# Performance work log

Hardware: AMD Instinct MI355X
Metric: run time of the kernel (lower is better)

## Reference

```python
import jax, jax.numpy as jnp
import numpy as np

B, D, C = 16384, 1024, 2048


def setup_inputs() -> dict:
    key = jax.random.key(0)
    k1, k2 = jax.random.split(key)
    x = jax.random.normal(k1, (B, D), dtype=jnp.float32)
    # xavier_uniform for centers of shape (C, D): bound = sqrt(6/(C+D))
    bound = float(np.sqrt(6.0 / (C + D)))
    centers = jax.random.uniform(k2, (C, D), dtype=jnp.float32, minval=-bound, maxval=bound)
    gamma = jnp.ones((1,), dtype=jnp.float32)
    return {"x": x, "centers": centers, "gamma": gamma}


def _rbf(x, centers, gamma):
    # then Euclidean norm (sqrt) and exp(-gamma * dist) as in the torch module.
    x2 = jnp.sum(x * x, axis=-1, keepdims=True)            # (B, 1)
    c2 = jnp.sum(centers * centers, axis=-1)               # (C,)
    sq = x2 - 2.0 * jnp.einsum('bd,cd->bc', x, centers) + c2[None, :]
    dist = jnp.sqrt(jnp.maximum(sq, 0.0))                  # (B, C)
    return jnp.exp(-gamma[0] * dist)


def reference(x, centers, gamma):
    return _rbf(x, centers, gamma)
```

## Files before the change

### kernel.cpp

```cpp
#include <hip/hip_runtime.h>
#include <stdint.h>


typedef __attribute__((ext_vector_type(4))) int i32x4;

#define BM 128
#define BN 128
#define BK 64

__global__ __launch_bounds__(256) void prep_i8(
    const float* __restrict__ in, unsigned char* __restrict__ qb,
    float2* __restrict__ info, int K) {
  int row = blockIdx.x;
  int tid = threadIdx.x;
  float4 v = ((const float4*)(in + (size_t)row * K))[tid];
  float ss = v.x * v.x + v.y * v.y + v.z * v.z + v.w * v.w;
  float am = fmaxf(fmaxf(fabsf(v.x), fabsf(v.y)), fmaxf(fabsf(v.z), fabsf(v.w)));
  for (int off = 32; off > 0; off >>= 1) {
    ss += __shfl_down(ss, off, 64);
    am = fmaxf(am, __shfl_down(am, off, 64));
  }
  __shared__ float pss[4], pam[4], sbc;
  int lane = tid & 63, w = tid >> 6;
  if (lane == 0) { pss[w] = ss; pam[w] = am; }
  __syncthreads();
  if (tid == 0) {
    float tss = pss[0] + pss[1] + pss[2] + pss[3];
    float tam = fmaxf(fmaxf(pam[0], pam[1]), fmaxf(pam[2], pam[3]));
    float s = tam > 0.f ? 127.f / tam : 0.f;
    info[row] = make_float2(tss, tam * (1.f / 127.f));
    sbc = s;
  }
  __syncthreads();
  float s = sbc;
  int qx = __float2int_rn(v.x * s), qy = __float2int_rn(v.y * s);
  int qz = __float2int_rn(v.z * s), qw = __float2int_rn(v.w * s);
  unsigned u = (unsigned)(qx & 255) | ((unsigned)(qy & 255) << 8) |
               ((unsigned)(qz & 255) << 16) | ((unsigned)(qw & 255) << 24);
  ((unsigned*)qb)[(size_t)row * (K >> 2) + tid] = u;
}

#define GLDS(gptr, lptr)                                                      \
  __builtin_amdgcn_global_load_lds(                                           \
      (const __attribute__((address_space(1))) unsigned int*)(gptr),          \
      (__attribute__((address_space(3))) unsigned int*)(lptr), 16, 0, 0)

#define DSR(dst, addr, imm)                                                   \
  asm volatile("ds_read_b128 %0, %1 offset:%c2"                              \
               : "=v"(dst) : "v"(addr), "i"(imm))

#define BARRIER __builtin_amdgcn_s_barrier()
#define LGKM0                                                                 \
  do {                                                                        \
    asm volatile("s_waitcnt lgkmcnt(0)" ::: "memory");                        \
    __builtin_amdgcn_sched_barrier(0);                                        \
  } while (0)
#define VMW(n) asm volatile("s_waitcnt vmcnt(" #n ")" ::: "memory")

#define MFMAI8(a, b, c) __builtin_amdgcn_mfma_i32_16x16x64_i8((a), (b), (c), 0, 0, 0)

__global__ __launch_bounds__(256) void rbf_gemm_i8(
    const unsigned char* __restrict__ A, const unsigned char* __restrict__ Bm,
    const float2* __restrict__ xinfo, const float2* __restrict__ cinfo,
    const float* __restrict__ gamma, float* __restrict__ out,
    int M, int N, int K) {
  __shared__ __align__(16) unsigned char lds[2 * 16384];

  int nbn = N / BN;
  int nwg = (M / BM) * nbn;
  int bid = blockIdx.x;
  int wg = bid;
  if ((nwg & 7) == 0) {
    int cpx = nwg >> 3;
    wg = (bid & 7) * cpx + (bid >> 3);
  }
  int bm = wg / nbn, bn = wg % nbn;

  int tid = threadIdx.x;
  int lane = tid & 63, wv = tid >> 6;
  int wm = wv >> 1;
  int wn = wv & 1;
  int l15 = lane & 15, l4 = lane >> 4;

  const size_t Kz = (size_t)K;

  int pr = tid >> 2;
  int lr = pr ^ ((pr >> 2) & 1);
  int ls = (tid & 3) ^ (lr & 3);
  const unsigned char* AgT = A + (size_t)bm * BM * Kz + (size_t)lr * Kz + ls * 16;
  const unsigned char* BgT = Bm + (size_t)bn * BN * Kz + (size_t)lr * Kz + ls * 16;
  size_t rstep = (size_t)64 * Kz;

#define STG4(TAU, BUFS)                                                       \
  do {                                                                        \
    GLDS(AgT + (size_t)(TAU) * 64, (BUFS) + tid * 16);                        \
    GLDS(AgT + rstep + (size_t)(TAU) * 64, (BUFS) + 4096 + tid * 16);         \
    GLDS(BgT + (size_t)(TAU) * 64, (BUFS) + 8192 + tid * 16);                 \
    GLDS(BgT + rstep + (size_t)(TAU) * 64, (BUFS) + 12288 + tid * 16);        \
  } while (0)

  int sl15 = l15 ^ ((l15 >> 2) & 1);
  int fsl = l4 ^ (l15 & 3);
  unsigned ldsBase =
      (unsigned)(size_t)(const __attribute__((address_space(3))) void*)&lds[0];
  unsigned aBase = ldsBase + (unsigned)(wm * 4096 + sl15 * 64 + fsl * 16);
  unsigned bBase = ldsBase + (unsigned)(8192 + wn * 4096 + sl15 * 64 + fsl * 16);

  i32x4 acc[4][4];
#pragma unroll
  for (int m = 0; m < 4; ++m)
#pragma unroll
    for (int n = 0; n < 4; ++n) acc[m][n] = (i32x4){0, 0, 0, 0};

  int nt = K / BK;

  STG4(0, lds);
  VMW(0);
  BARRIER;

  for (int t = 0; t < nt; ++t) {
    unsigned bufOff = (unsigned)(t & 1) * 16384u;
    unsigned char* bufS = lds + ((t + 1) & 1) * 16384;

    unsigned aAd = aBase + bufOff;
    unsigned bAd = bBase + bufOff;

    i32x4 a0, a1, a2, a3, b0, b1, b2, b3;
    DSR(a0, aAd, 0);    DSR(a1, aAd, 1024);
    DSR(a2, aAd, 2048); DSR(a3, aAd, 3072);
    DSR(b0, bAd, 0);    DSR(b1, bAd, 1024);
    DSR(b2, bAd, 2048); DSR(b3, bAd, 3072);
    if (t + 1 < nt) STG4(t + 1, bufS);
    LGKM0;
    __builtin_amdgcn_s_setprio(1);
    acc[0][0] = MFMAI8(a0, b0, acc[0][0]);
    acc[0][1] = MFMAI8(a0, b1, acc[0][1]);
    acc[0][2] = MFMAI8(a0, b2, acc[0][2]);
    acc[0][3] = MFMAI8(a0, b3, acc[0][3]);
    acc[1][0] = MFMAI8(a1, b0, acc[1][0]);
    acc[1][1] = MFMAI8(a1, b1, acc[1][1]);
    acc[1][2] = MFMAI8(a1, b2, acc[1][2]);
    acc[1][3] = MFMAI8(a1, b3, acc[1][3]);
    acc[2][0] = MFMAI8(a2, b0, acc[2][0]);
    acc[2][1] = MFMAI8(a2, b1, acc[2][1]);
    acc[2][2] = MFMAI8(a2, b2, acc[2][2]);
    acc[2][3] = MFMAI8(a2, b3, acc[2][3]);
    acc[3][0] = MFMAI8(a3, b0, acc[3][0]);
    acc[3][1] = MFMAI8(a3, b1, acc[3][1]);
    acc[3][2] = MFMAI8(a3, b2, acc[3][2]);
    acc[3][3] = MFMAI8(a3, b3, acc[3][3]);
    __builtin_amdgcn_s_setprio(0);

    if (t < nt - 1) {
      VMW(0);
      BARRIER;
    }
  }

  float g = gamma[0];
  int rb0 = bm * BM + wm * 64 + l4 * 4;
  int cb0 = bn * BN + wn * 64 + l15;
#pragma unroll
  for (int m = 0; m < 4; ++m) {
#pragma unroll
    for (int j = 0; j < 4; ++j) {
      int row = rb0 + m * 16 + j;
      float2 xi = xinfo[row];
      size_t ob = (size_t)row * N;
#pragma unroll
      for (int n = 0; n < 4; ++n) {
        int col = cb0 + n * 16;
        float2 ci = cinfo[col];
        float dot = (float)acc[m][n][j] * xi.y * ci.y;
        float sq = fmaxf(xi.x + ci.x - 2.f * dot, 0.f);
        out[ob + col] = __expf(-g * __builtin_sqrtf(sq));
      }
    }
  }
}

__global__ __launch_bounds__(256) void rbf_naive(
    const float* __restrict__ x, const float* __restrict__ cent,
    const float* __restrict__ gamma, float* __restrict__ out, int D, int N) {
  int row = blockIdx.x;
  int col = blockIdx.y * blockDim.x + threadIdx.x;
  extern __shared__ float xs[];
  for (int i = threadIdx.x; i < D; i += blockDim.x)
    xs[i] = x[(size_t)row * D + i];
  __syncthreads();
  if (col >= N) return;
  const float* cp = cent + (size_t)col * D;
  float s = 0.f;
  for (int d = 0; d < D; ++d) {
    float df = xs[d] - cp[d];
    s += df * df;
  }
  out[(size_t)row * N + col] = __expf(-gamma[0] * __builtin_sqrtf(fmaxf(s, 0.f)));
}

extern "C" void kernel_launch(void* const* d_in, const int* in_sizes, int n_in,
                              void* d_out, int out_size, void* d_ws, size_t ws_size,
                              hipStream_t stream) {
  const float* x = (const float*)d_in[0];
  const float* cent = (const float*)d_in[1];
  const float* gamma = (const float*)d_in[2];
  float* out = (float*)d_out;

  const int D = 1024;
  int Brows = in_sizes[0] / D;
  int C = in_sizes[1] / D;

  size_t qa = (size_t)Brows * D;
  size_t qc = (size_t)C * D;
  size_t need = qa + qc + (size_t)Brows * 8 + (size_t)C * 8;
  bool can = (ws_size >= need) && (D == 1024) && (Brows % BM == 0) &&
             (C % BN == 0);

  if (!can) {
    dim3 grid(Brows, (C + 255) / 256);
    hipLaunchKernelGGL(rbf_naive, grid, dim3(256), D * sizeof(float), stream,
                       x, cent, gamma, out, D, C);
    return;
  }

  unsigned char* xb = (unsigned char*)d_ws;
  unsigned char* cb = xb + qa;
  float2* xinfo = (float2*)(xb + qa + qc);
  float2* cinfo = xinfo + Brows;

  hipLaunchKernelGGL(prep_i8, dim3(Brows), dim3(256), 0, stream, x, xb, xinfo, D);
  hipLaunchKernelGGL(prep_i8, dim3(C), dim3(256), 0, stream, cent, cb, cinfo, D);

  int nwg = (Brows / BM) * (C / BN);
  hipLaunchKernelGGL(rbf_gemm_i8, dim3(nwg), dim3(256), 0, stream,
                     xb, cb, xinfo, cinfo, gamma, out, Brows, C, D);
}
```

Before: 93.74 us.

## Replace LDS-staged int8 GEMM loads with direct global-to-register double buffering

The int8 MFMA mainloop no longer stages A/B tiles through shared memory with global_load_lds and barriers. Each wave now loads its own fragments straight from global memory into registers with global_load_dwordx4, ping-ponging two register sets across a fully unrolled K loop. This removes LDS traffic and workgroup barriers. In exchange, waves sharing rows or columns now fetch duplicate data from global or L2, and the per-row access pattern is less coalesced.

```diff
diff --git a/kernel.cpp b/kernel.cpp
--- a/kernel.cpp
+++ b/kernel.cpp
@@ -6,7 +6,7 @@
 
 #define BM 128
 #define BN 128
-#define BK 64
+#define KDIM 1024
 
 __global__ __launch_bounds__(256) void prep_i8(
     const float* __restrict__ in, unsigned char* __restrict__ qb,
@@ -40,22 +40,15 @@
   ((unsigned*)qb)[(size_t)row * (K >> 2) + tid] = u;
 }
 
-#define GLDS(gptr, lptr)                                                      \
-  __builtin_amdgcn_global_load_lds(                                           \
-      (const __attribute__((address_space(1))) unsigned int*)(gptr),          \
-      (__attribute__((address_space(3))) unsigned int*)(lptr), 16, 0, 0)
-
-#define DSR(dst, addr, imm)                                                   \
-  asm volatile("ds_read_b128 %0, %1 offset:%c2"                              \
-               : "=v"(dst) : "v"(addr), "i"(imm))
-
-#define BARRIER __builtin_amdgcn_s_barrier()
-#define LGKM0                                                                 \
-  do {                                                                        \
-    asm volatile("s_waitcnt lgkmcnt(0)" ::: "memory");                        \
+#define GLD(dst, ptr, imm)                                                    \
+  asm volatile("global_load_dwordx4 %0, %1, off offset:%c2"                  \
+               : "=v"(dst) : "v"(ptr), "i"(imm))
+
+#define VMW(n)                                                                \
+  do {                                                                        \
+    asm volatile("s_waitcnt vmcnt(" #n ")" ::: "memory");                     \
     __builtin_amdgcn_sched_barrier(0);                                        \
   } while (0)
-#define VMW(n) asm volatile("s_waitcnt vmcnt(" #n ")" ::: "memory")
 
 #define MFMAI8(a, b, c) __builtin_amdgcn_mfma_i32_16x16x64_i8((a), (b), (c), 0, 0, 0)
 
@@ -63,9 +56,7 @@
     const unsigned char* __restrict__ A, const unsigned char* __restrict__ Bm,
     const float2* __restrict__ xinfo, const float2* __restrict__ cinfo,
     const float* __restrict__ gamma, float* __restrict__ out,
-    int M, int N, int K) {
-  __shared__ __align__(16) unsigned char lds[2 * 16384];
-
+    int M, int N) {
   int nbn = N / BN;
   int nwg = (M / BM) * nbn;
   int bid = blockIdx.x;
@@ -82,29 +73,16 @@
   int wn = wv & 1;
   int l15 = lane & 15, l4 = lane >> 4;
 
-  const size_t Kz = (size_t)K;
-
-  int pr = tid >> 2;
-  int lr = pr ^ ((pr >> 2) & 1);
-  int ls = (tid & 3) ^ (lr & 3);
-  const unsigned char* AgT = A + (size_t)bm * BM * Kz + (size_t)lr * Kz + ls * 16;
-  const unsigned char* BgT = Bm + (size_t)bn * BN * Kz + (size_t)lr * Kz + ls * 16;
-  size_t rstep = (size_t)64 * Kz;
-
-#define STG4(TAU, BUFS)                                                       \
-  do {                                                                        \
-    GLDS(AgT + (size_t)(TAU) * 64, (BUFS) + tid * 16);                        \
-    GLDS(AgT + rstep + (size_t)(TAU) * 64, (BUFS) + 4096 + tid * 16);         \
-    GLDS(BgT + (size_t)(TAU) * 64, (BUFS) + 8192 + tid * 16);                 \
-    GLDS(BgT + rstep + (size_t)(TAU) * 64, (BUFS) + 12288 + tid * 16);        \
-  } while (0)
-
-  int sl15 = l15 ^ ((l15 >> 2) & 1);
-  int fsl = l4 ^ (l15 & 3);
-  unsigned ldsBase =
-      (unsigned)(size_t)(const __attribute__((address_space(3))) void*)&lds[0];
-  unsigned aBase = ldsBase + (unsigned)(wm * 4096 + sl15 * 64 + fsl * 16);
-  unsigned bBase = ldsBase + (unsigned)(8192 + wn * 4096 + sl15 * 64 + fsl * 16);
+  const unsigned char* pA0 =
+      A + (size_t)(bm * BM + wm * 64 + l15) * KDIM + l4 * 16;
+  const unsigned char* pA1 = pA0 + (size_t)16 * KDIM;
+  const unsigned char* pA2 = pA0 + (size_t)32 * KDIM;
+  const unsigned char* pA3 = pA0 + (size_t)48 * KDIM;
+  const unsigned char* pB0 =
+      Bm + (size_t)(bn * BN + wn * 64 + l15) * KDIM + l4 * 16;
+  const unsigned char* pB1 = pB0 + (size_t)16 * KDIM;
+  const unsigned char* pB2 = pB0 + (size_t)32 * KDIM;
+  const unsigned char* pB3 = pB0 + (size_t)48 * KDIM;
 
   i32x4 acc[4][4];
 #pragma unroll
@@ -112,49 +90,56 @@
 #pragma unroll
     for (int n = 0; n < 4; ++n) acc[m][n] = (i32x4){0, 0, 0, 0};
 
-  int nt = K / BK;
-
-  STG4(0, lds);
-  VMW(0);
-  BARRIER;
-
-  for (int t = 0; t < nt; ++t) {
-    unsigned bufOff = (unsigned)(t & 1) * 16384u;
-    unsigned char* bufS = lds + ((t + 1) & 1) * 16384;
-
-    unsigned aAd = aBase + bufOff;
-    unsigned bAd = bBase + bufOff;
-
-    i32x4 a0, a1, a2, a3, b0, b1, b2, b3;
-    DSR(a0, aAd, 0);    DSR(a1, aAd, 1024);
-    DSR(a2, aAd, 2048); DSR(a3, aAd, 3072);
-    DSR(b0, bAd, 0);    DSR(b1, bAd, 1024);
-    DSR(b2, bAd, 2048); DSR(b3, bAd, 3072);
-    if (t + 1 < nt) STG4(t + 1, bufS);
-    LGKM0;
-    __builtin_amdgcn_s_setprio(1);
-    acc[0][0] = MFMAI8(a0, b0, acc[0][0]);
-    acc[0][1] = MFMAI8(a0, b1, acc[0][1]);
-    acc[0][2] = MFMAI8(a0, b2, acc[0][2]);
-    acc[0][3] = MFMAI8(a0, b3, acc[0][3]);
-    acc[1][0] = MFMAI8(a1, b0, acc[1][0]);
-    acc[1][1] = MFMAI8(a1, b1, acc[1][1]);
-    acc[1][2] = MFMAI8(a1, b2, acc[1][2]);
-    acc[1][3] = MFMAI8(a1, b3, acc[1][3]);
-    acc[2][0] = MFMAI8(a2, b0, acc[2][0]);
-    acc[2][1] = MFMAI8(a2, b1, acc[2][1]);
-    acc[2][2] = MFMAI8(a2, b2, acc[2][2]);
-    acc[2][3] = MFMAI8(a2, b3, acc[2][3]);
-    acc[3][0] = MFMAI8(a3, b0, acc[3][0]);
-    acc[3][1] = MFMAI8(a3, b1, acc[3][1]);
-    acc[3][2] = MFMAI8(a3, b2, acc[3][2]);
-    acc[3][3] = MFMAI8(a3, b3, acc[3][3]);
-    __builtin_amdgcn_s_setprio(0);
-
-    if (t < nt - 1) {
+  i32x4 a0, a1, a2, a3, b0, b1, b2, b3;
+  i32x4 a4, a5, a6, a7, b4, b5, b6, b7;
+
+#define LOAD_S0(OFF)                                                          \
+  do {                                                                        \
+    GLD(a0, pA0, OFF); GLD(a1, pA1, OFF); GLD(a2, pA2, OFF); GLD(a3, pA3, OFF); \
+    GLD(b0, pB0, OFF); GLD(b1, pB1, OFF); GLD(b2, pB2, OFF); GLD(b3, pB3, OFF); \
+  } while (0)
+#define LOAD_S1(OFF)                                                          \
+  do {                                                                        \
+    GLD(a4, pA0, OFF); GLD(a5, pA1, OFF); GLD(a6, pA2, OFF); GLD(a7, pA3, OFF); \
+    GLD(b4, pB0, OFF); GLD(b5, pB1, OFF); GLD(b6, pB2, OFF); GLD(b7, pB3, OFF); \
+  } while (0)
+
+#define MFMA_S0()                                                             \
+  do {                                                                        \
+    acc[0][0] = MFMAI8(a0, b0, acc[0][0]); acc[0][1] = MFMAI8(a0, b1, acc[0][1]); \
+    acc[0][2] = MFMAI8(a0, b2, acc[0][2]); acc[0][3] = MFMAI8(a0, b3, acc[0][3]); \
+    acc[1][0] = MFMAI8(a1, b0, acc[1][0]); acc[1][1] = MFMAI8(a1, b1, acc[1][1]); \
+    acc[1][2] = MFMAI8(a1, b2, acc[1][2]); acc[1][3] = MFMAI8(a1, b3, acc[1][3]); \
+    acc[2][0] = MFMAI8(a2, b0, acc[2][0]); acc[2][1] = MFMAI8(a2, b1, acc[2][1]); \
+    acc[2][2] = MFMAI8(a2, b2, acc[2][2]); acc[2][3] = MFMAI8(a2, b3, acc[2][3]); \
+    acc[3][0] = MFMAI8(a3, b0, acc[3][0]); acc[3][1] = MFMAI8(a3, b1, acc[3][1]); \
+    acc[3][2] = MFMAI8(a3, b2, acc[3][2]); acc[3][3] = MFMAI8(a3, b3, acc[3][3]); \
+  } while (0)
+#define MFMA_S1()                                                             \
+  do {                                                                        \
+    acc[0][0] = MFMAI8(a4, b4, acc[0][0]); acc[0][1] = MFMAI8(a4, b5, acc[0][1]); \
+    acc[0][2] = MFMAI8(a4, b6, acc[0][2]); acc[0][3] = MFMAI8(a4, b7, acc[0][3]); \
+    acc[1][0] = MFMAI8(a5, b4, acc[1][0]); acc[1][1] = MFMAI8(a5, b5, acc[1][1]); \
+    acc[1][2] = MFMAI8(a5, b6, acc[1][2]); acc[1][3] = MFMAI8(a5, b7, acc[1][3]); \
+    acc[2][0] = MFMAI8(a6, b4, acc[2][0]); acc[2][1] = MFMAI8(a6, b5, acc[2][1]); \
+    acc[2][2] = MFMAI8(a6, b6, acc[2][2]); acc[2][3] = MFMAI8(a6, b7, acc[2][3]); \
+    acc[3][0] = MFMAI8(a7, b4, acc[3][0]); acc[3][1] = MFMAI8(a7, b5, acc[3][1]); \
+    acc[3][2] = MFMAI8(a7, b6, acc[3][2]); acc[3][3] = MFMAI8(a7, b7, acc[3][3]); \
+  } while (0)
+
+  LOAD_S0(0);
+#pragma unroll
+  for (int tp = 0; tp < 8; ++tp) {
+    LOAD_S1((2 * tp + 1) * 64);
+    VMW(8);
+    MFMA_S0();
+    if (tp < 7) {
+      LOAD_S0((2 * tp + 2) * 64);
+      VMW(8);
+    } else {
       VMW(0);
-      BARRIER;
     }
+    MFMA_S1();
   }
 
   float g = gamma[0];
@@ -233,5 +218,5 @@
 
   int nwg = (Brows / BM) * (C / BN);
   hipLaunchKernelGGL(rbf_gemm_i8, dim3(nwg), dim3(256), 0, stream,
-                     xb, cb, xinfo, cinfo, gamma, out, Brows, C, D);
-}
+                     xb, cb, xinfo, cinfo, gamma, out, Brows, C);
+}
```

Result: slower. 161.5 us (+72.3%).
